# Kernel tuning notes

Measured on AMD Instinct MI355X. Metric: run time of the kernel, lower is better.

The kernel has to match this reference:

```python
import jax, jax.numpy as jnp
import numpy as np
import math

EMBED_DIM = 1024
NUM_HEADS = 16
HEAD_DIM = EMBED_DIM // NUM_HEADS
B, S = 2, 2048


def setup_inputs() -> dict:
    key = jax.random.key(0)
    ks = jax.random.split(key, 13)
    sc = 1.0 / math.sqrt(EMBED_DIM)
    inp = {
        "query": jax.random.normal(ks[0], (B, S, EMBED_DIM), jnp.float32),
        "key": jax.random.normal(ks[1], (B, S, EMBED_DIM), jnp.float32),
        "value": jax.random.normal(ks[2], (B, S, EMBED_DIM), jnp.float32),
        "input_patch_mask": jax.random.randint(ks[3], (B, S), 0, 2, jnp.int32),
        "Wq": jax.random.normal(ks[4], (EMBED_DIM, EMBED_DIM), jnp.float32) * sc,
        "bq": jnp.zeros((EMBED_DIM,), jnp.float32),
        "Wk": jax.random.normal(ks[5], (EMBED_DIM, EMBED_DIM), jnp.float32) * sc,
        "bk": jnp.zeros((EMBED_DIM,), jnp.float32),
        "Wv": jax.random.normal(ks[6], (EMBED_DIM, EMBED_DIM), jnp.float32) * sc,
        "bv": jnp.zeros((EMBED_DIM,), jnp.float32),
        "Wo": jax.random.normal(ks[7], (EMBED_DIM, EMBED_DIM), jnp.float32) * sc,
        "bo": jnp.zeros((EMBED_DIM,), jnp.float32),
    }
    return inp


def _masked_softmax(scores, mask):
    # Equivalent to masked_fill(-inf) -> softmax -> nan_to_num(0.0):
    # fully-masked rows produce exactly 0, without generating NaNs.
    neg_inf = jnp.array(-jnp.inf, scores.dtype)
    s = jnp.where(mask, scores, neg_inf)
    m = jnp.max(s, axis=-1, keepdims=True)
    m_safe = jnp.where(jnp.isfinite(m), m, jnp.zeros_like(m))
    e = jnp.where(mask, jnp.exp(s - m_safe), 0.0)
    denom = jnp.sum(e, axis=-1, keepdims=True)
    denom = jnp.where(denom == 0.0, 1.0, denom)
    return e / denom


def reference(query, key, value, input_patch_mask, Wq, bq, Wk, bk, Wv, bv, Wo, bo):
    b, s, d = query.shape
    h, hd = NUM_HEADS, HEAD_DIM
    q = (query @ Wq.T + bq).reshape(b, s, h, hd).transpose(0, 2, 1, 3)  # [b,h,s,hd]
    k = (key @ Wk.T + bk).reshape(b, s, h, hd).transpose(0, 2, 1, 3)
    v = (value @ Wv.T + bv).reshape(b, s, h, hd).transpose(0, 2, 1, 3)
    scores = jnp.einsum("bhqd,bhkd->bhqk", q, k) / math.sqrt(hd)
    # mask[b,i,j] = patch_mask[b,i] * patch_mask[b,j]
    mask = (input_patch_mask[:, :, None] * input_patch_mask[:, None, :]) > 0
    attn = _masked_softmax(scores, mask[:, None, :, :])  # dropout in eval mode = identity
    context = jnp.einsum("bhqk,bhkd->bhqd", attn, v)
    context = context.transpose(0, 2, 1, 3).reshape(b, s, d)
    return context @ Wo.T + bo
```

## Files before the change

### kernel.cpp

```cpp
#include <hip/hip_runtime.h>
#include <cstdint>
#include <cstddef>

#define EMBED 1024
#define NHEAD 16
#define HD    64
#define BATCH 2
#define SEQ   2048
#define MROWS (BATCH*SEQ)
#define QSCALE 0.1803368801111137f

typedef __bf16 bf16;
typedef __bf16 bf16x8 __attribute__((ext_vector_type(8)));
typedef float  f32x4  __attribute__((ext_vector_type(4)));
typedef unsigned int u32;

#if __has_builtin(__builtin_amdgcn_exp2f)
#define EXP2(x) __builtin_amdgcn_exp2f(x)
#else
#define EXP2(x) exp2f(x)
#endif

typedef const u32 __attribute__((address_space(1)))* gp_t;
typedef u32 __attribute__((address_space(3)))* lp_t;

__device__ __forceinline__ void g2l16(const void* g, void* l) {
  __builtin_amdgcn_global_load_lds((gp_t)(uintptr_t)g, (lp_t)(u32)(uintptr_t)l, 16, 0, 0);
}

#define MFMA(a, b, c) __builtin_amdgcn_mfma_f32_16x16x32_bf16((a), (b), (c), 0, 0, 0)

__global__ void cast_multi(const float* __restrict__ p0, const float* __restrict__ p1,
                           const float* __restrict__ p2, const float* __restrict__ p3,
                           bf16* o0, bf16* o1, bf16* o2, bf16* o3, int n8) {
  int z = blockIdx.y;
  const float* in = z==0?p0 : z==1?p1 : z==2?p2 : p3;
  bf16*       out = z==0?o0 : z==1?o1 : z==2?o2 : o3;
  int i = blockIdx.x * blockDim.x + threadIdx.x;
  if (i >= n8) return;
  const float4* p = (const float4*)in;
  float4 a = p[2*i], b = p[2*i+1];
  union { bf16 h[8]; uint4 u; } r;
  r.h[0] = (bf16)a.x; r.h[1] = (bf16)a.y; r.h[2] = (bf16)a.z; r.h[3] = (bf16)a.w;
  r.h[4] = (bf16)b.x; r.h[5] = (bf16)b.y; r.h[6] = (bf16)b.z; r.h[7] = (bf16)b.w;
  ((uint4*)out)[i] = r.u;
}

#define BM 128
#define BN 128
#define BK 32
#define NKI (EMBED/BK)

__device__ __forceinline__ void gemm_core(
    const bf16* __restrict__ A, const bf16* __restrict__ W,
    bf16* Al, bf16* Bl, f32x4 (&acc)[4][4])
{
  const int tid  = threadIdx.x;
  const int lane = tid & 63, wid = tid >> 6;
  const int quad = lane >> 4, l16 = lane & 15;
  const int wm = wid >> 1, wn = wid & 1;
  const int m0 = blockIdx.y * BM, n0 = blockIdx.x * BN;

  const int R = tid >> 2, Cc = tid & 3;
  const int gcol = (Cc ^ ((R >> 1) & 3)) * 8;
  const bf16* Ag = A + (size_t)(m0 + R) * EMBED + gcol;
  const bf16* Bg = W + (size_t)(n0 + R) * EMBED + gcol;
  bf16* AlW = Al + wid * 512;
  bf16* BlW = Bl + wid * 512;

  g2l16(Ag, AlW);                      g2l16(Ag + (size_t)64*EMBED, AlW + 2048);
  g2l16(Bg, BlW);                      g2l16(Bg + (size_t)64*EMBED, BlW + 2048);
  __syncthreads();

  for (int ki = 0; ki < NKI; ++ki) {
    const int cur = ki & 1;
    if (ki + 1 < NKI) {
      const int nb = cur ^ 1;
      const int k0 = (ki + 1) * BK;
      g2l16(Ag + k0, AlW + nb*4096);
      g2l16(Ag + (size_t)64*EMBED + k0, AlW + nb*4096 + 2048);
      g2l16(Bg + k0, BlW + nb*4096);
      g2l16(Bg + (size_t)64*EMBED + k0, BlW + nb*4096 + 2048);
    }
    const bf16* Ac = Al + cur*4096;
    const bf16* Bc = Bl + cur*4096;
    bf16x8 af[4], bg[4];
#pragma unroll
    for (int i = 0; i < 4; ++i) {
      int ra = wm*64 + i*16 + l16;
      af[i] = *(const bf16x8*)(Ac + ra*32 + ((quad ^ ((ra>>1)&3))*8));
      int rb = wn*64 + i*16 + l16;
      bg[i] = *(const bf16x8*)(Bc + rb*32 + ((quad ^ ((rb>>1)&3))*8));
    }
#pragma unroll
    for (int i = 0; i < 4; ++i)
#pragma unroll
      for (int j = 0; j < 4; ++j)
        acc[i][j] = MFMA(af[i], bg[j], acc[i][j]);
    __syncthreads();
  }
}

__global__ __launch_bounds__(256) void qkv_kernel(
    const bf16* __restrict__ Xq, const bf16* __restrict__ Xk, const bf16* __restrict__ Xv,
    const bf16* __restrict__ Wq, const bf16* __restrict__ Wk, const bf16* __restrict__ Wv,
    const float* __restrict__ bq, const float* __restrict__ bk, const float* __restrict__ bv,
    bf16* __restrict__ Qp, bf16* __restrict__ Kp, bf16* __restrict__ VTg)
{
  __shared__ bf16 Al[2*BM*BK];
  __shared__ bf16 Bl[2*BN*BK];
  const int z = blockIdx.z;
  const bf16* A = z==0 ? Xq : z==1 ? Xk : Xv;
  const bf16* W = z==0 ? Wq : z==1 ? Wk : Wv;
  const float* bias = z==0 ? bq : z==1 ? bk : bv;
  const float scale = (z==0) ? QSCALE : 1.0f;

  f32x4 acc[4][4] = {};
  gemm_core(A, W, Al, Bl, acc);

  const int lane = threadIdx.x & 63, wid = threadIdx.x >> 6;
  const int quad = lane >> 4, l16 = lane & 15;
  const int wm = wid >> 1, wn = wid & 1;
  const int m0 = blockIdx.y * BM, n0 = blockIdx.x * BN;

#pragma unroll
  for (int i = 0; i < 4; ++i) {
#pragma unroll
    for (int j = 0; j < 4; ++j) {
      int col = n0 + wn*64 + j*16 + l16;
      float bv2 = bias[col];
      if (z < 2) {
        bf16* outp = (z == 0) ? Qp : Kp;
#pragma unroll
        for (int r = 0; r < 4; ++r) {
          int row = m0 + wm*64 + i*16 + quad*4 + r;
          outp[(size_t)row*EMBED + col] = (bf16)((acc[i][j][r] + bv2) * scale);
        }
      } else {
        int row0 = m0 + wm*64 + i*16 + quad*4;
        int bb = row0 >> 11, ss = row0 & (SEQ-1);
        int hh = col >> 6, dd = col & (HD-1);
        union { bf16 h4[4]; uint2 u; } pk;
#pragma unroll
        for (int r = 0; r < 4; ++r) pk.h4[r] = (bf16)(acc[i][j][r] + bv2);
        *(uint2*)(VTg + (((size_t)bb*NHEAD + hh)*HD + dd)*SEQ + ss) = pk.u;
      }
    }
  }
}

__global__ __launch_bounds__(256) void oproj_kernel(
    const bf16* __restrict__ Ctx, const bf16* __restrict__ Wo,
    const float* __restrict__ bo, float* __restrict__ out)
{
  __shared__ bf16 Al[2*128*32];
  __shared__ bf16 Bl[2*64*32];
  const int tid  = threadIdx.x;
  const int lane = tid & 63, wid = tid >> 6;
  const int quad = lane >> 4, l16 = lane & 15;
  const int m0 = blockIdx.y * 128, n0 = blockIdx.x * 64;

  const int R = tid >> 2, Cc = tid & 3;
  const int gcol = (Cc ^ ((R >> 1) & 3)) * 8;
  const bf16* Ag = Ctx + (size_t)(m0 + R) * EMBED + gcol;
  const bf16* Bg = Wo  + (size_t)(n0 + R) * EMBED + gcol;
  bf16* AlW = Al + wid * 512;
  bf16* BlW = Bl + wid * 512;

  g2l16(Ag, AlW);  g2l16(Ag + (size_t)64*EMBED, AlW + 2048);
  g2l16(Bg, BlW);
  __syncthreads();

  f32x4 acc[2][4] = {};
  for (int ki = 0; ki < NKI; ++ki) {
    const int cur = ki & 1;
    if (ki + 1 < NKI) {
      const int nb = cur ^ 1;
      const int k0 = (ki + 1) * BK;
      g2l16(Ag + k0, AlW + nb*4096);
      g2l16(Ag + (size_t)64*EMBED + k0, AlW + nb*4096 + 2048);
      g2l16(Bg + k0, BlW + nb*2048);
    }
    const bf16* Ac = Al + cur*4096;
    const bf16* Bc = Bl + cur*2048;
    bf16x8 af[2], bg[4];
#pragma unroll
    for (int u = 0; u < 2; ++u) {
      int ra = wid*32 + u*16 + l16;
      af[u] = *(const bf16x8*)(Ac + ra*32 + ((quad ^ ((ra>>1)&3))*8));
    }
#pragma unroll
    for (int j = 0; j < 4; ++j) {
      int rb = j*16 + l16;
      bg[j] = *(const bf16x8*)(Bc + rb*32 + ((quad ^ ((rb>>1)&3))*8));
    }
#pragma unroll
    for (int u = 0; u < 2; ++u)
#pragma unroll
      for (int j = 0; j < 4; ++j)
        acc[u][j] = MFMA(af[u], bg[j], acc[u][j]);
    __syncthreads();
  }

#pragma unroll
  for (int u = 0; u < 2; ++u)
#pragma unroll
    for (int j = 0; j < 4; ++j) {
      int col = n0 + j*16 + l16;
      float bv = bo[col];
#pragma unroll
      for (int r = 0; r < 4; ++r) {
        int row = m0 + wid*32 + u*16 + quad*4 + r;
        out[(size_t)row*EMBED + col] = (acc[u][j][r] + bv);
      }
    }
}

#define NT  (SEQ/64)
#define PST 68

__global__ __launch_bounds__(256, 3) void attn_kernel(
    const bf16* __restrict__ Qp, const bf16* __restrict__ Kp, const bf16* __restrict__ VT,
    const int* __restrict__ pmask, bf16* __restrict__ Ctx)
{
  __shared__ bf16 Kt[2][64*64];
  __shared__ bf16 Vt[2][64*64];
  __shared__ bf16 Pl[4][32*PST];

  const int qt = blockIdx.x, h = blockIdx.y, b = blockIdx.z;
  const int tid = threadIdx.x, lane = tid & 63, wid = tid >> 6;
  const int quad = lane >> 4, l16 = lane & 15;
  const int qrow0 = qt*128 + wid*32;

  bf16x8 qf[2][2];
#pragma unroll
  for (int u = 0; u < 2; ++u) {
    const size_t qoff = (size_t)(b*SEQ + qrow0 + u*16 + l16)*EMBED + h*HD;
    qf[u][0] = *(const bf16x8*)(Qp + qoff + quad*8);
    qf[u][1] = *(const bf16x8*)(Qp + qoff + 32 + quad*8);
  }

  int qm[2][4];
#pragma unroll
  for (int u = 0; u < 2; ++u)
#pragma unroll
    for (int r = 0; r < 4; ++r) qm[u][r] = pmask[b*SEQ + qrow0 + u*16 + quad*4 + r];

  bf16 onev = (bf16)1.0f;
  bf16x8 ones = {onev, onev, onev, onev, onev, onev, onev, onev};

  const bf16* Kg  = Kp + (size_t)b*SEQ*EMBED + h*HD;
  const bf16* VTg = VT + (size_t)(b*NHEAD + h)*HD*SEQ;

  const int R = tid >> 3;
  const int Cc = tid & 7;
  const int scol = (Cc ^ (R & 7)) * 8;

  f32x4 o[2][4] = {};
  f32x4 lacc[2] = {};

#define STAGE(kt, buf) do {                                              \
    const bf16* kg = Kg + (size_t)((kt)*64 + R)*EMBED + scol;            \
    const bf16* vg = VTg + (size_t)R*SEQ + (kt)*64 + scol;               \
    bf16* kl = &Kt[buf][0] + wid*512;                                    \
    bf16* vl = &Vt[buf][0] + wid*512;                                    \
    g2l16(kg, kl);  g2l16(kg + (size_t)32*EMBED, kl + 2048);             \
    g2l16(vg, vl);  g2l16(vg + (size_t)32*SEQ,   vl + 2048);             \
  } while (0)

  STAGE(0, 0);
  __syncthreads();

  for (int kt = 0; kt < NT; ++kt) {
    const int cur = kt & 1;
    if (kt + 1 < NT) STAGE(kt + 1, cur ^ 1);
    const bf16* Kc = &Kt[cur][0];
    const bf16* Vc = &Vt[cur][0];

#pragma unroll
    for (int g = 0; g < 4; ++g) {
      int ra = g*16 + l16, sa = ra & 7;
      bf16x8 kfa = *(const bf16x8*)(Kc + ra*64 + ((quad     ^ sa)*8));
      bf16x8 kfb = *(const bf16x8*)(Kc + ra*64 + (((quad+4) ^ sa)*8));
      int km = pmask[b*SEQ + kt*64 + g*16 + l16];
#pragma unroll
      for (int u = 0; u < 2; ++u) {
        f32x4 sg = {};
        sg = MFMA(qf[u][0], kfa, sg);
        sg = MFMA(qf[u][1], kfb, sg);
#pragma unroll
        for (int r = 0; r < 4; ++r) {
          float pv = km ? EXP2(sg[r]) : 0.0f;
          Pl[wid][(u*16 + quad*4 + r)*PST + g*16 + l16] = (bf16)pv;
        }
      }
    }

    bf16x8 pf[2][2];
#pragma unroll
    for (int u = 0; u < 2; ++u) {
      pf[u][0] = *(const bf16x8*)(&Pl[wid][(u*16 + l16)*PST + quad*8]);
      pf[u][1] = *(const bf16x8*)(&Pl[wid][(u*16 + l16)*PST + 32 + quad*8]);
      lacc[u] = MFMA(pf[u][0], ones, lacc[u]);
      lacc[u] = MFMA(pf[u][1], ones, lacc[u]);
    }
#pragma unroll
    for (int t = 0; t < 4; ++t) {
      int rd = t*16 + l16, sd = rd & 7;
      bf16x8 vf0 = *(const bf16x8*)(Vc + rd*64 + ((quad     ^ sd)*8));
      bf16x8 vf1 = *(const bf16x8*)(Vc + rd*64 + (((quad+4) ^ sd)*8));
#pragma unroll
      for (int u = 0; u < 2; ++u) {
        o[u][t] = MFMA(pf[u][0], vf0, o[u][t]);
        o[u][t] = MFMA(pf[u][1], vf1, o[u][t]);
      }
    }
    __syncthreads();
  }

#pragma unroll
  for (int u = 0; u < 2; ++u) {
    float inv[4];
#pragma unroll
    for (int r = 0; r < 4; ++r)
      inv[r] = (qm[u][r] && lacc[u][r] > 0.f) ? 1.0f / lacc[u][r] : 0.0f;
#pragma unroll
    for (int t = 0; t < 4; ++t)
#pragma unroll
      for (int r = 0; r < 4; ++r) {
        int row = b*SEQ + qrow0 + u*16 + quad*4 + r;
        Ctx[(size_t)row*EMBED + h*HD + t*16 + l16] = (bf16)(o[u][t][r] * inv[r]);
      }
  }
}

extern "C" void kernel_launch(void* const* d_in, const int* in_sizes, int n_in,
                              void* d_out, int out_size, void* d_ws, size_t ws_size,
                              hipStream_t stream)
{
  const float* query = (const float*)d_in[0];
  const float* key   = (const float*)d_in[1];
  const float* value = (const float*)d_in[2];
  const int*   pm    = (const int*)d_in[3];
  const float* Wq = (const float*)d_in[4];
  const float* bq = (const float*)d_in[5];
  const float* Wk = (const float*)d_in[6];
  const float* bk = (const float*)d_in[7];
  const float* Wv = (const float*)d_in[8];
  const float* bv = (const float*)d_in[9];
  const float* Wo = (const float*)d_in[10];
  const float* bo = (const float*)d_in[11];
  float* out = (float*)d_out;

  const size_t SZ_X = (size_t)MROWS * EMBED;
  const size_t SZ_W = (size_t)EMBED * EMBED;

  bf16* p   = (bf16*)d_ws;
  bf16* Xq  = p; p += SZ_X;
  bf16* Xk  = p; p += SZ_X;
  bf16* Xv  = p; p += SZ_X;
  bf16* Wqb = p; p += SZ_W;
  bf16* Wkb = p; p += SZ_W;
  bf16* Wvb = p; p += SZ_W;
  bf16* Wob = p; p += SZ_W;
  bf16* Qp  = p; p += SZ_X;
  bf16* Kp  = p; p += SZ_X;
  bf16* VTg = p; p += SZ_X;
  bf16* Ctx = p; p += SZ_X;

  dim3 gx((unsigned)(SZ_X/8/256), 3);
  cast_multi<<<gx, 256, 0, stream>>>(query, key, value, query, Xq, Xk, Xv, Xq, (int)(SZ_X/8));
  dim3 gw((unsigned)(SZ_W/8/256), 4);
  cast_multi<<<gw, 256, 0, stream>>>(Wq, Wk, Wv, Wo, Wqb, Wkb, Wvb, Wob, (int)(SZ_W/8));

  dim3 gq(EMBED/BN, MROWS/BM, 3);
  qkv_kernel<<<gq, 256, 0, stream>>>(Xq, Xk, Xv, Wqb, Wkb, Wvb, bq, bk, bv, Qp, Kp, VTg);

  dim3 ga(SEQ/128, NHEAD, BATCH);
  attn_kernel<<<ga, 256, 0, stream>>>(Qp, Kp, VTg, pm, Ctx);

  dim3 gg(EMBED/64, MROWS/128);
  oproj_kernel<<<gg, 256, 0, stream>>>(Ctx, Wob, bo, out);
}
```

Baseline: 237.3 us.

## Permute V^T key order to vectorize P stores, merge cast kernels

The V-projection epilogue now writes V^T with keys permuted inside each 64-key tile, so that the attention kernel can pack each lane's four exp values across key groups into one 8-byte shared-memory store instead of four scalar bf16 stores. The P row stride changes from 68 to 72 to keep those vector stores aligned. The two fp32-to-bf16 cast launches are merged into one seven-slice launch to save a kernel launch. The price is scalar scattered global writes for V^T in the QKV epilogue, plus more live registers for the stored score fragments.

```diff
diff --git a/kernel.cpp b/kernel.cpp
--- a/kernel.cpp
+++ b/kernel.cpp
@@ -30,12 +30,27 @@
 
 #define MFMA(a, b, c) __builtin_amdgcn_mfma_f32_16x16x32_bf16((a), (b), (c), 0, 0, 0)
 
-__global__ void cast_multi(const float* __restrict__ p0, const float* __restrict__ p1,
-                           const float* __restrict__ p2, const float* __restrict__ p3,
-                           bf16* o0, bf16* o1, bf16* o2, bf16* o3, int n8) {
+#define SZX8 ((MROWS*EMBED)/8)
+#define SZW8 ((EMBED*EMBED)/8)
+
+__global__ void cast_all(const float* __restrict__ q, const float* __restrict__ k,
+                         const float* __restrict__ v, const float* __restrict__ wq,
+                         const float* __restrict__ wk, const float* __restrict__ wv,
+                         const float* __restrict__ wo,
+                         bf16* xq, bf16* xk, bf16* xv,
+                         bf16* wqb, bf16* wkb, bf16* wvb, bf16* wob) {
   int z = blockIdx.y;
-  const float* in = z==0?p0 : z==1?p1 : z==2?p2 : p3;
-  bf16*       out = z==0?o0 : z==1?o1 : z==2?o2 : o3;
+  const float* in; bf16* out;
+  switch (z) {
+    case 0: in = q;  out = xq;  break;
+    case 1: in = k;  out = xk;  break;
+    case 2: in = v;  out = xv;  break;
+    case 3: in = wq; out = wqb; break;
+    case 4: in = wk; out = wkb; break;
+    case 5: in = wv; out = wvb; break;
+    default: in = wo; out = wob; break;
+  }
+  int n8 = (z < 3) ? SZX8 : SZW8;
   int i = blockIdx.x * blockDim.x + threadIdx.x;
   if (i >= n8) return;
   const float4* p = (const float4*)in;
@@ -138,12 +153,16 @@
         }
       } else {
         int row0 = m0 + wm*64 + i*16 + quad*4;
-        int bb = row0 >> 11, ss = row0 & (SEQ-1);
+        int bb = row0 >> 11, ss0 = row0 & (SEQ-1);
         int hh = col >> 6, dd = col & (HD-1);
-        union { bf16 h4[4]; uint2 u; } pk;
-#pragma unroll
-        for (int r = 0; r < 4; ++r) pk.h4[r] = (bf16)(acc[i][j][r] + bv2);
-        *(uint2*)(VTg + (((size_t)bb*NHEAD + hh)*HD + dd)*SEQ + ss) = pk.u;
+        const size_t base = (((size_t)bb*NHEAD + hh)*HD + dd)*SEQ;
+#pragma unroll
+        for (int r = 0; r < 4; ++r) {
+          int s = ss0 + r;
+          int tile = s >> 6, loc = s & 63;
+          int p = ((loc & 15) << 2) | (loc >> 4);
+          VTg[base + tile*64 + p] = (bf16)(acc[i][j][r] + bv2);
+        }
       }
     }
   }
@@ -217,7 +236,7 @@
 }
 
 #define NT  (SEQ/64)
-#define PST 68
+#define PST 72
 
 __global__ __launch_bounds__(256, 3) void attn_kernel(
     const bf16* __restrict__ Qp, const bf16* __restrict__ Kp, const bf16* __restrict__ VT,
@@ -277,6 +296,7 @@
     const bf16* Kc = &Kt[cur][0];
     const bf16* Vc = &Vt[cur][0];
 
+    f32x4 sg[2][4];
 #pragma unroll
     for (int g = 0; g < 4; ++g) {
       int ra = g*16 + l16, sa = ra & 7;
@@ -285,16 +305,23 @@
       int km = pmask[b*SEQ + kt*64 + g*16 + l16];
 #pragma unroll
       for (int u = 0; u < 2; ++u) {
-        f32x4 sg = {};
-        sg = MFMA(qf[u][0], kfa, sg);
-        sg = MFMA(qf[u][1], kfb, sg);
-#pragma unroll
-        for (int r = 0; r < 4; ++r) {
-          float pv = km ? EXP2(sg[r]) : 0.0f;
-          Pl[wid][(u*16 + quad*4 + r)*PST + g*16 + l16] = (bf16)pv;
-        }
-      }
-    }
+        f32x4 s = {};
+        s = MFMA(qf[u][0], kfa, s);
+        s = MFMA(qf[u][1], kfb, s);
+#pragma unroll
+        for (int r = 0; r < 4; ++r) sg[u][g][r] = km ? EXP2(s[r]) : 0.0f;
+      }
+    }
+
+#pragma unroll
+    for (int u = 0; u < 2; ++u)
+#pragma unroll
+      for (int r = 0; r < 4; ++r) {
+        union { bf16 h[4]; uint2 uu; } pk;
+#pragma unroll
+        for (int g = 0; g < 4; ++g) pk.h[g] = (bf16)sg[u][g][r];
+        *(uint2*)(&Pl[wid][(u*16 + quad*4 + r)*PST + l16*4]) = pk.uu;
+      }
 
     bf16x8 pf[2][2];
 #pragma unroll
@@ -368,10 +395,9 @@
   bf16* VTg = p; p += SZ_X;
   bf16* Ctx = p; p += SZ_X;
 
-  dim3 gx((unsigned)(SZ_X/8/256), 3);
-  cast_multi<<<gx, 256, 0, stream>>>(query, key, value, query, Xq, Xk, Xv, Xq, (int)(SZ_X/8));
-  dim3 gw((unsigned)(SZ_W/8/256), 4);
-  cast_multi<<<gw, 256, 0, stream>>>(Wq, Wk, Wv, Wo, Wqb, Wkb, Wvb, Wob, (int)(SZ_W/8));
+  dim3 gc((unsigned)(SZX8/256), 7);
+  cast_all<<<gc, 256, 0, stream>>>(query, key, value, Wq, Wk, Wv, Wo,
+                                   Xq, Xk, Xv, Wqb, Wkb, Wvb, Wob);
 
   dim3 gq(EMBED/BN, MROWS/BM, 3);
   qkv_kernel<<<gq, 256, 0, stream>>>(Xq, Xk, Xv, Wqb, Wkb, Wvb, bq, bk, bv, Qp, Kp, VTg);
```

New measurement: 234.7 us. About the same (-1.1%).
